# Kernel tuning notes

Hardware: AMD Instinct MI355X
Metric: run time of the kernel (lower is better)

Reference implementation:

```python
import jax, jax.numpy as jnp
import numpy as np

B, L, H, D = 1, 2048, 24, 128
BLKQ = BLKK = 64
TOPK_RATIO = 0.5


def setup_inputs() -> dict:
    key = jax.random.key(0)
    kq, kk, kv, kw = jax.random.split(key, 4)
    q = jax.random.normal(kq, (B, L, H, D), jnp.float32)
    k = jax.random.normal(kk, (B, L, H, D), jnp.float32)
    v = jax.random.normal(kv, (B, L, H, D), jnp.float32)
    proj_w = jax.random.normal(kw, (D, D), jnp.float32) * 0.02  # nn.Linear weight (out,in)
    proj_b = jnp.zeros((D,), jnp.float32)
    return {"query": q, "key": k, "value": v, "proj_w": proj_w, "proj_b": proj_b}


def _block_sparse_attention(q, k, v, scale):
    # q,k,v: (B,H,L,D). Block-mean pooled QK scores pick top-k key blocks per query block.
    Nq, Nk = L // BLKQ, L // BLKK
    topk = max(1, int(Nk * TOPK_RATIO))  # real_topk
    qb = q.reshape(B, H, Nq, BLKQ, D).mean(axis=3)          # (B,H,Nq,D)
    kb = k.reshape(B, H, Nk, BLKK, D).mean(axis=3)          # (B,H,Nk,D)
    blk_scores = jnp.einsum('bhqd,bhkd->bhqk', qb, kb)      # pooled block map
    _, lut = jax.lax.top_k(blk_scores, topk)                # (B,H,Nq,topk) selected key blocks
    kblk = k.reshape(B, H, Nk, BLKK, D)
    vblk = v.reshape(B, H, Nk, BLKK, D)
    idx = lut.reshape(B, H, Nq * topk, 1, 1)
    kg = jnp.take_along_axis(kblk, idx, axis=2).reshape(B, H, Nq, topk * BLKK, D)
    vg = jnp.take_along_axis(vblk, idx, axis=2).reshape(B, H, Nq, topk * BLKK, D)
    qr = q.reshape(B, H, Nq, BLKQ, D)
    scores = jnp.einsum('bhqid,bhqjd->bhqij', qr, kg) * scale  # (B,H,Nq,BLKQ,topk*BLKK)
    attn = jax.nn.softmax(scores, axis=-1)
    o = jnp.einsum('bhqij,bhqjd->bhqid', attn, vg)
    return o.reshape(B, H, L, D)


def _linear_attention(q, k, v):
    # feature_map='softmax' over the head dim
    ql = jax.nn.softmax(q, axis=-1)
    kl = jax.nn.softmax(k, axis=-1)
    kvsum = jnp.einsum('bhld,bhle->bhde', kl, v)            # K^T V  (B,H,D,D)
    ksum = kl.sum(axis=2)                                    # (B,H,D)
    num = jnp.einsum('bhld,bhde->bhle', ql, kvsum)
    den = 1e-5 + jnp.einsum('bhld,bhd->bhl', ql, ksum)[..., None]
    return num / den


def reference(query, key, value, proj_w, proj_b):
    q = jnp.swapaxes(query, 1, 2)  # (B,H,L,D)
    k = jnp.swapaxes(key, 1, 2)
    v = jnp.swapaxes(value, 1, 2)
    scale = D ** -0.5  # softmax_scale = head_size**-0.5
    o_s = _block_sparse_attention(q, k, v, scale)
    o_l = _linear_attention(q, k, v)
    o_l = o_l @ proj_w.T + proj_b  # learnable fusion projection
    out = jnp.swapaxes(o_s + o_l, 1, 2)  # back to (B,L,H,D)
    return out
```

## Files before the change

kernel.cpp:

```cpp
#include <hip/hip_runtime.h>
#include <math.h>

#define HH 24
#define LLEN 2048
#define DD 128
#define BLK 64
#define NBLK 32
#define TOPK 16
#define NCHUNK 16

typedef __attribute__((ext_vector_type(8))) short bf16x8;
typedef __attribute__((ext_vector_type(4))) float f32x4;

typedef unsigned int u32_g __attribute__((address_space(1)));
typedef unsigned int u32_l __attribute__((address_space(3)));

__device__ __forceinline__ unsigned short f2bf(float f) {
    unsigned u = __builtin_bit_cast(unsigned, f);
    unsigned r = (u + 0x7FFFu + ((u >> 16) & 1u)) >> 16;
    return (unsigned short)r;
}
__device__ __forceinline__ float bf2f(unsigned short b) {
    unsigned u = ((unsigned)b) << 16;
    return __builtin_bit_cast(float, u);
}
__device__ __forceinline__ void gload16(unsigned short* lds, const unsigned short* g) {
    __builtin_amdgcn_global_load_lds((const u32_g*)g, (u32_l*)lds, 16, 0, 0);
}

__global__ __launch_bounds__(256) void convert_pool(
    const float* __restrict__ q, const float* __restrict__ k, const float* __restrict__ v,
    unsigned short* __restrict__ kb16, unsigned short* __restrict__ vt16,
    float* __restrict__ qb, float* __restrict__ kb)
{
    const int nb = blockIdx.x, h = blockIdx.y;
    const int l0 = nb * BLK;
    const int tid = threadIdx.x;
    __shared__ unsigned short vt_s[DD * BLK];

    {
        const int r = tid >> 2, c0 = (tid & 3) * 4;
        const float* kp = k + ((size_t)(l0 + r) * HH + h) * DD + c0 * 8;
        unsigned short* krow = kb16 + ((size_t)h * LLEN + l0 + r) * DD;
        #pragma unroll
        for (int j = 0; j < 4; ++j) {
            float4 a = *(const float4*)(kp + j * 8);
            float4 c = *(const float4*)(kp + j * 8 + 4);
            unsigned short tmp[8] = {f2bf(a.x), f2bf(a.y), f2bf(a.z), f2bf(a.w),
                                     f2bf(c.x), f2bf(c.y), f2bf(c.z), f2bf(c.w)};
            const int chunk = (c0 + j) ^ (r & 7);
            *(bf16x8*)&krow[chunk * 8] = *(bf16x8*)tmp;
        }
    }
    {
        const int kp2 = tid >> 3, dgb = tid & 7;
        const float* v0p = v + ((size_t)(l0 + kp2 * 2) * HH + h) * DD;
        const float* v1p = v0p + (size_t)HH * DD;
        #pragma unroll
        for (int j2 = 0; j2 < 4; ++j2) {
            const int d0 = dgb * 4 + j2 * 32;
            float4 a = *(const float4*)(v0p + d0);
            float4 c = *(const float4*)(v1p + d0);
            float a4[4] = {a.x, a.y, a.z, a.w}, c4[4] = {c.x, c.y, c.z, c.w};
            #pragma unroll
            for (int i = 0; i < 4; ++i) {
                unsigned pak = (unsigned)f2bf(a4[i]) | ((unsigned)f2bf(c4[i]) << 16);
                const int d = d0 + i;
                const int chunk = (kp2 >> 2) ^ (d & 7);
                *(unsigned*)&vt_s[d * BLK + chunk * 8 + (kp2 & 3) * 2] = pak;
            }
        }
    }
    __syncthreads();
    {
        bf16x8* dstv = (bf16x8*)(vt16 + (size_t)(h * NBLK + nb) * DD * BLK);
        const bf16x8* srcv = (const bf16x8*)vt_s;
        #pragma unroll
        for (int j = 0; j < 4; ++j) dstv[tid * 4 + j] = srcv[tid * 4 + j];
    }
    __syncthreads();
    {
        float* ps = (float*)vt_s;
        const int d = tid & 127, half = tid >> 7;
        const size_t rs = (size_t)HH * DD;
        const float* qp = q + ((size_t)(l0 + half * 32) * HH + h) * DD + d;
        const float* kp = k + ((size_t)(l0 + half * 32) * HH + h) * DD + d;
        float sq = 0.f, sk = 0.f;
        #pragma unroll 8
        for (int i = 0; i < 32; ++i) { sq += qp[i * rs]; sk += kp[i * rs]; }
        ps[half * 128 + d] = sq;
        ps[256 + half * 128 + d] = sk;
        __syncthreads();
        if (half == 0) {
            qb[((size_t)h * NBLK + nb) * DD + d] = ps[d] + ps[128 + d];
            kb[((size_t)h * NBLK + nb) * DD + d] = ps[256 + d] + ps[384 + d];
        }
    }
}

__global__ __launch_bounds__(256) void topk_kernel(
    const float* __restrict__ qb, const float* __restrict__ kb, int* __restrict__ lut)
{
    const int h = blockIdx.x;
    __shared__ float kb_s[NBLK][DD];
    __shared__ float sc[NBLK][NBLK];
    const int tid = threadIdx.x;
    for (int f = tid; f < NBLK * DD / 4; f += 256)
        ((float4*)kb_s)[f] = ((const float4*)(kb + (size_t)h * NBLK * DD))[f];
    __syncthreads();
    for (int p = tid; p < NBLK * NBLK; p += 256) {
        const int iq = p >> 5, ik = p & 31;
        const float4* qr4 = (const float4*)(qb + ((size_t)h * NBLK + iq) * DD);
        const float4* kr4 = (const float4*)&kb_s[ik][0];
        float s = 0.f;
        for (int dq = 0; dq < DD / 4; ++dq) {
            float4 a = qr4[dq], b = kr4[dq];
            s += a.x * b.x + a.y * b.y + a.z * b.z + a.w * b.w;
        }
        sc[iq][ik] = s;
    }
    __syncthreads();
    if (tid < NBLK) {
        const int iq = tid;
        for (int t = 0; t < TOPK; ++t) {
            float bv = -1e30f; int bi = 0;
            for (int j = 0; j < NBLK; ++j) {
                float s = sc[iq][j];
                if (s > bv) { bv = s; bi = j; }
            }
            lut[((size_t)h * NBLK + iq) * TOPK + t] = bi;
            sc[iq][bi] = -1e30f;
        }
    }
}

__global__ __launch_bounds__(256, 2) void kv_mfma(
    const float* __restrict__ k, const unsigned short* __restrict__ vt16,
    float* __restrict__ kvp, float* __restrict__ ksp)
{
    const int h = blockIdx.x, c = blockIdx.y;
    __shared__ unsigned short klT[DD * DD];
    const int tid = threadIdx.x;
    const int quad = tid >> 3, dpart = tid & 7;
    const int d0 = dpart * 16;
    const int wid = tid >> 6, lane = tid & 63;
    const int l15 = lane & 15, g = lane >> 4;

    f32x4 acc[2][8];
    #pragma unroll
    for (int mi = 0; mi < 2; ++mi)
        #pragma unroll
        for (int nt = 0; nt < 8; ++nt) acc[mi][nt] = (f32x4){0.f, 0.f, 0.f, 0.f};
    float ksa[16];
    #pragma unroll
    for (int j = 0; j < 16; ++j) ksa[j] = 0.f;

    const int l0 = c * DD;
    {
        const int lr = quad * 4;
        float rows[4][16];
        #pragma unroll
        for (int i = 0; i < 4; ++i) {
            const float4* kp4 = (const float4*)(k + ((size_t)(l0 + lr + i) * HH + h) * DD + d0);
            #pragma unroll
            for (int t4 = 0; t4 < 4; ++t4) {
                float4 x = kp4[t4];
                rows[i][t4 * 4 + 0] = x.x; rows[i][t4 * 4 + 1] = x.y;
                rows[i][t4 * 4 + 2] = x.z; rows[i][t4 * 4 + 3] = x.w;
            }
        }
        #pragma unroll
        for (int i = 0; i < 4; ++i) {
            float mx = -1e30f;
            #pragma unroll
            for (int j = 0; j < 16; ++j) mx = fmaxf(mx, rows[i][j]);
            mx = fmaxf(mx, __shfl_xor(mx, 1));
            mx = fmaxf(mx, __shfl_xor(mx, 2));
            mx = fmaxf(mx, __shfl_xor(mx, 4));
            float s = 0.f;
            #pragma unroll
            for (int j = 0; j < 16; ++j) { rows[i][j] = __expf(rows[i][j] - mx); s += rows[i][j]; }
            s += __shfl_xor(s, 1);
            s += __shfl_xor(s, 2);
            s += __shfl_xor(s, 4);
            const float rinv = 1.0f / s;
            #pragma unroll
            for (int j = 0; j < 16; ++j) { rows[i][j] *= rinv; ksa[j] += rows[i][j]; }
        }
        #pragma unroll
        for (int j = 0; j < 16; ++j) {
            const int d = d0 + j;
            unsigned long long pk =
                (unsigned long long)f2bf(rows[0][j]) |
                ((unsigned long long)f2bf(rows[1][j]) << 16) |
                ((unsigned long long)f2bf(rows[2][j]) << 32) |
                ((unsigned long long)f2bf(rows[3][j]) << 48);
            const int chunk = (quad >> 1) ^ (d & 7);
            *(unsigned long long*)&klT[d * DD + chunk * 8 + (quad & 1) * 4] = pk;
        }
    }
    __syncthreads();
    const int bkt = c * 2;
    #pragma unroll
    for (int ks = 0; ks < 4; ++ks) {
        bf16x8 af[2];
        #pragma unroll
        for (int mi = 0; mi < 2; ++mi) {
            const int d = (wid * 2 + mi) * 16 + l15;
            const int chunk = (ks * 4 + g) ^ (d & 7);
            af[mi] = *(const bf16x8*)&klT[d * DD + chunk * 8];
        }
        const int s = ks * 4 + g;
        const int kt = bkt + (s >> 3);
        #pragma unroll
        for (int nt = 0; nt < 8; ++nt) {
            const int e = nt * 16 + l15;
            const int cc = (s & 7) ^ (e & 7);
            bf16x8 bf = *(const bf16x8*)&vt16[((size_t)(h * NBLK + kt) * DD + e) * BLK + cc * 8];
            acc[0][nt] = __builtin_amdgcn_mfma_f32_16x16x32_bf16(af[0], bf, acc[0][nt], 0, 0, 0);
            acc[1][nt] = __builtin_amdgcn_mfma_f32_16x16x32_bf16(af[1], bf, acc[1][nt], 0, 0, 0);
        }
    }
    float* op = kvp + ((size_t)h * NCHUNK + c) * DD * DD;
    #pragma unroll
    for (int mi = 0; mi < 2; ++mi)
        #pragma unroll
        for (int nt = 0; nt < 8; ++nt)
            #pragma unroll
            for (int r = 0; r < 4; ++r)
                op[(size_t)((wid * 2 + mi) * 16 + g * 4 + r) * DD + nt * 16 + l15] = acc[mi][nt][r];
    #pragma unroll
    for (int j = 0; j < 16; ++j) {
        ksa[j] += __shfl_xor(ksa[j], 8);
        ksa[j] += __shfl_xor(ksa[j], 16);
        ksa[j] += __shfl_xor(ksa[j], 32);
    }
    if ((lane >> 3) == 0) {
        float* kp2 = ksp + (((size_t)h * NCHUNK + c) * 4 + wid) * DD + d0;
        #pragma unroll
        for (int j = 0; j < 16; ++j) kp2[j] = ksa[j];
    }
}

__global__ __launch_bounds__(256) void reduce_M(
    const float* __restrict__ kvp, const float* __restrict__ ksp,
    const float* __restrict__ W, unsigned short* __restrict__ Mt,
    float* __restrict__ ksumf)
{
    const int h = blockIdx.x, rb = blockIdx.y;
    __shared__ float kv_s[32][DD];
    const int tid = threadIdx.x;
    for (int f4 = tid; f4 < 32 * DD / 4; f4 += 256) {
        float4 s = make_float4(0.f, 0.f, 0.f, 0.f);
        #pragma unroll
        for (int cc = 0; cc < NCHUNK; ++cc) {
            float4 x = ((const float4*)(kvp + ((size_t)h * NCHUNK + cc) * DD * DD
                                        + (size_t)rb * 32 * DD))[f4];
            s.x += x.x; s.y += x.y; s.z += x.z; s.w += x.w;
        }
        ((float4*)kv_s)[f4] = s;
    }
    if (rb == 0 && tid < DD) {
        float s = 0.f;
        #pragma unroll
        for (int p = 0; p < NCHUNK * 4; ++p)
            s += ksp[((size_t)h * NCHUNK * 4 + p) * DD + tid];
        ksumf[(size_t)h * DD + tid] = s;
    }
    __syncthreads();
    const int e = tid & 127, dh = tid >> 7;
    float accm[16];
    #pragma unroll
    for (int i = 0; i < 16; ++i) accm[i] = 0.f;
    const float4* wr4 = (const float4*)(W + (size_t)e * DD);
    for (int c4 = 0; c4 < DD / 4; ++c4) {
        const float4 wv = wr4[c4];
        #pragma unroll
        for (int i = 0; i < 16; ++i) {
            const float4 kv4 = ((const float4*)&kv_s[dh * 16 + i][0])[c4];
            accm[i] += kv4.x * wv.x + kv4.y * wv.y + kv4.z * wv.z + kv4.w * wv.w;
        }
    }
    unsigned short* mp = Mt + (size_t)h * DD * DD + (size_t)e * DD + rb * 32 + dh * 16;
    #pragma unroll
    for (int ii = 0; ii < 16; ii += 2) {
        unsigned pk = (unsigned)f2bf(accm[ii]) | ((unsigned)f2bf(accm[ii + 1]) << 16);
        *(unsigned*)&mp[ii] = pk;
    }
}

__global__ __launch_bounds__(256, 2) void sla_attn(
    const float* __restrict__ q, const unsigned short* __restrict__ kb16,
    const unsigned short* __restrict__ vt16, const int* __restrict__ lut,
    const unsigned short* __restrict__ Mt, const float* __restrict__ ksumf,
    const float* __restrict__ pb, float* __restrict__ out)
{
    const int b = blockIdx.x;
    const int slot = b >> 3;
    const int h = (b & 7) + 8 * (slot >> 5);
    const int nq = slot & 31;

    __shared__ unsigned short Ks[2][BLK * DD];
    __shared__ unsigned short Vt[2][DD * BLK];
    __shared__ unsigned short Ps[4 * 16 * BLK];

    const int tid = threadIdx.x;
    const int wid = tid >> 6, lane = tid & 63;
    const int l15 = lane & 15, g = lane >> 4;
    const int q0 = wid * 16;

    bf16x8 qhi[4], qlo[4];
    {
        const float scale = 0.08838834764831845f;
        const int qrow = nq * BLK + q0 + l15;
        const float* qp = q + ((size_t)qrow * HH + h) * DD;
        #pragma unroll
        for (int ks = 0; ks < 4; ++ks) {
            const int d0 = ks * 32 + g * 8;
            float4 a = *(const float4*)(qp + d0);
            float4 c = *(const float4*)(qp + d0 + 4);
            float vv[8] = {a.x, a.y, a.z, a.w, c.x, c.y, c.z, c.w};
            #pragma unroll
            for (int j = 0; j < 8; ++j) {
                float s = vv[j] * scale;
                unsigned short hi = f2bf(s);
                float lo = s - bf2f(hi);
                qhi[ks][j] = (short)hi;
                qlo[ks][j] = (short)f2bf(lo);
            }
        }
    }

    f32x4 Oacc[8];
    #pragma unroll
    for (int nt = 0; nt < 8; ++nt) Oacc[nt] = (f32x4){0.f, 0.f, 0.f, 0.f};
    float m_run = -1e30f, l_run = 0.f;

    const int* lrow = lut + ((size_t)h * NBLK + nq) * TOPK;

    {
        const int kbI = lrow[0];
        const unsigned short* kg = kb16 + ((size_t)h * LLEN + (size_t)kbI * BLK) * DD;
        const unsigned short* vg = vt16 + (size_t)(h * NBLK + kbI) * DD * BLK;
        #pragma unroll
        for (int i = 0; i < 4; ++i) {
            const int is = wid * 4 + i;
            gload16(&Ks[0][is * 512], kg + is * 512 + lane * 8);
            gload16(&Vt[0][is * 512], vg + is * 512 + lane * 8);
        }
    }
    __syncthreads();

    for (int it = 0; it < TOPK; ++it) {
        const int cur = it & 1;
        if (it + 1 < TOPK) {
            const int kbN = lrow[it + 1];
            const unsigned short* kg = kb16 + ((size_t)h * LLEN + (size_t)kbN * BLK) * DD;
            const unsigned short* vg = vt16 + (size_t)(h * NBLK + kbN) * DD * BLK;
            #pragma unroll
            for (int i = 0; i < 4; ++i) {
                const int is = wid * 4 + i;
                gload16(&Ks[cur ^ 1][is * 512], kg + is * 512 + lane * 8);
                gload16(&Vt[cur ^ 1][is * 512], vg + is * 512 + lane * 8);
            }
        }
        const unsigned short* KsC = &Ks[cur][0];
        const unsigned short* VtC = &Vt[cur][0];

        f32x4 sacc[4];
        #pragma unroll
        for (int mt = 0; mt < 4; ++mt) sacc[mt] = (f32x4){0.f, 0.f, 0.f, 0.f};
        #pragma unroll
        for (int ks = 0; ks < 4; ++ks) {
            #pragma unroll
            for (int mt = 0; mt < 4; ++mt) {
                const int row = mt * 16 + l15;
                const int chunk = (ks * 4 + g) ^ (row & 7);
                bf16x8 kf = *(const bf16x8*)&KsC[row * DD + chunk * 8];
                sacc[mt] = __builtin_amdgcn_mfma_f32_16x16x32_bf16(kf, qhi[ks], sacc[mt], 0, 0, 0);
                sacc[mt] = __builtin_amdgcn_mfma_f32_16x16x32_bf16(kf, qlo[ks], sacc[mt], 0, 0, 0);
            }
        }

        float sv[16];
        #pragma unroll
        for (int mt = 0; mt < 4; ++mt)
            #pragma unroll
            for (int r = 0; r < 4; ++r) sv[mt * 4 + r] = sacc[mt][r];
        float mx = -1e30f;
        #pragma unroll
        for (int i = 0; i < 16; ++i) mx = fmaxf(mx, sv[i]);
        mx = fmaxf(mx, __shfl_xor(mx, 16));
        mx = fmaxf(mx, __shfl_xor(mx, 32));
        const float mnew = fmaxf(m_run, mx);
        const float alpha = __expf(m_run - mnew);
        float ssum = 0.f;
        #pragma unroll
        for (int i = 0; i < 16; ++i) { sv[i] = __expf(sv[i] - mnew); ssum += sv[i]; }
        ssum += __shfl_xor(ssum, 16);
        ssum += __shfl_xor(ssum, 32);
        l_run = l_run * alpha + ssum;
        m_run = mnew;

        {
            unsigned short* pw = Ps + wid * (16 * BLK) + l15 * BLK;
            #pragma unroll
            for (int mt = 0; mt < 4; ++mt) {
                #pragma unroll
                for (int pr = 0; pr < 2; ++pr) {
                    const int key = mt * 16 + g * 4 + pr * 2;
                    unsigned pak = (unsigned)f2bf(sv[mt * 4 + pr * 2])
                                 | ((unsigned)f2bf(sv[mt * 4 + pr * 2 + 1]) << 16);
                    const int chunk = (key >> 3) ^ (l15 & 7);
                    *(unsigned*)&pw[chunk * 8 + (key & 7)] = pak;
                }
            }
        }

        {
            float ar[4];
            #pragma unroll
            for (int r = 0; r < 4; ++r) ar[r] = __shfl(alpha, g * 4 + r);
            #pragma unroll
            for (int nt = 0; nt < 8; ++nt) {
                Oacc[nt][0] *= ar[0]; Oacc[nt][1] *= ar[1];
                Oacc[nt][2] *= ar[2]; Oacc[nt][3] *= ar[3];
            }
            const unsigned short* prd = Ps + wid * (16 * BLK) + l15 * BLK;
            #pragma unroll
            for (int ks2 = 0; ks2 < 2; ++ks2) {
                const int pch = (g + 4 * ks2) ^ (l15 & 7);
                bf16x8 pa = *(const bf16x8*)&prd[pch * 8];
                #pragma unroll
                for (int nt = 0; nt < 8; ++nt) {
                    const int drow = nt * 16 + l15;
                    const int vch = (g + 4 * ks2) ^ (drow & 7);
                    bf16x8 vf = *(const bf16x8*)&VtC[drow * BLK + vch * 8];
                    Oacc[nt] = __builtin_amdgcn_mfma_f32_16x16x32_bf16(pa, vf, Oacc[nt], 0, 0, 0);
                }
            }
        }
        __syncthreads();
    }

    float qv[32];
    {
        const float iscale = 11.313708498984761f;
        #pragma unroll
        for (int ks = 0; ks < 4; ++ks)
            #pragma unroll
            for (int j = 0; j < 8; ++j)
                qv[ks * 8 + j] = (bf2f((unsigned short)qhi[ks][j])
                                + bf2f((unsigned short)qlo[ks][j])) * iscale;
    }
    float mx2 = -1e30f;
    #pragma unroll
    for (int j = 0; j < 32; ++j) mx2 = fmaxf(mx2, qv[j]);
    mx2 = fmaxf(mx2, __shfl_xor(mx2, 16));
    mx2 = fmaxf(mx2, __shfl_xor(mx2, 32));
    float s2 = 0.f;
    #pragma unroll
    for (int j = 0; j < 32; ++j) { qv[j] = __expf(qv[j] - mx2); s2 += qv[j]; }
    s2 += __shfl_xor(s2, 16);
    s2 += __shfl_xor(s2, 32);
    const float rinv = 1.0f / s2;
    float den = 0.f;
    bf16x8 af[4];
    {
        const float* ksb = ksumf + (size_t)h * DD;
        #pragma unroll
        for (int ks = 0; ks < 4; ++ks) {
            const int dd0 = ks * 32 + g * 8;
            float4 k0 = *(const float4*)(ksb + dd0);
            float4 k1 = *(const float4*)(ksb + dd0 + 4);
            float kk[8] = {k0.x, k0.y, k0.z, k0.w, k1.x, k1.y, k1.z, k1.w};
            #pragma unroll
            for (int j = 0; j < 8; ++j) {
                const float ql = qv[ks * 8 + j] * rinv;
                af[ks][j] = (short)f2bf(ql);
                den += ql * kk[j];
            }
        }
    }
    den += __shfl_xor(den, 16);
    den += __shfl_xor(den, 32);
    const float dinv = 1.0f / (1e-5f + den);

    f32x4 acc2[8];
    #pragma unroll
    for (int nt = 0; nt < 8; ++nt) acc2[nt] = (f32x4){0.f, 0.f, 0.f, 0.f};
    {
        const unsigned short* mrow = Mt + (size_t)h * DD * DD;
        #pragma unroll
        for (int ks = 0; ks < 4; ++ks) {
            #pragma unroll
            for (int nt = 0; nt < 8; ++nt) {
                bf16x8 bf = *(const bf16x8*)&mrow[(size_t)(nt * 16 + l15) * DD + (ks * 4 + g) * 8];
                acc2[nt] = __builtin_amdgcn_mfma_f32_16x16x32_bf16(af[ks], bf, acc2[nt], 0, 0, 0);
            }
        }
    }

    float bias[8];
    #pragma unroll
    for (int nt = 0; nt < 8; ++nt) bias[nt] = pb[nt * 16 + l15];
    #pragma unroll
    for (int r = 0; r < 4; ++r) {
        const float linv = 1.0f / __shfl(l_run, g * 4 + r);
        const float di = __shfl(dinv, g * 4 + r);
        const int grow = nq * BLK + q0 + g * 4 + r;
        float* dst = out + ((size_t)grow * HH + h) * DD + l15;
        #pragma unroll
        for (int nt = 0; nt < 8; ++nt)
            dst[nt * 16] = Oacc[nt][r] * linv + acc2[nt][r] * di + bias[nt];
    }
}

extern "C" void kernel_launch(void* const* d_in, const int* in_sizes, int n_in,
                              void* d_out, int out_size, void* d_ws, size_t ws_size,
                              hipStream_t stream)
{
    (void)in_sizes; (void)n_in; (void)out_size; (void)ws_size;
    const float* q  = (const float*)d_in[0];
    const float* k  = (const float*)d_in[1];
    const float* v  = (const float*)d_in[2];
    const float* pw = (const float*)d_in[3];
    const float* pb = (const float*)d_in[4];
    float* out = (float*)d_out;
    char* ws = (char*)d_ws;
    size_t off = 0;
    int*   lut   = (int*)(ws + off);   off += (size_t)HH * NBLK * TOPK * 4;
    float* qb    = (float*)(ws + off); off += (size_t)HH * NBLK * DD * 4;
    float* kb    = (float*)(ws + off); off += (size_t)HH * NBLK * DD * 4;
    float* kvp   = (float*)(ws + off); off += (size_t)HH * NCHUNK * DD * DD * 4;
    float* ksp   = (float*)(ws + off); off += (size_t)HH * NCHUNK * 4 * DD * 4;
    unsigned short* Mt = (unsigned short*)(ws + off); off += (size_t)HH * DD * DD * 2;
    float* ksumf = (float*)(ws + off); off += (size_t)HH * DD * 4;
    unsigned short* kb16 = (unsigned short*)(ws + off); off += (size_t)HH * LLEN * DD * 2;
    unsigned short* vt16 = (unsigned short*)(ws + off); off += (size_t)HH * LLEN * DD * 2;

    convert_pool<<<dim3(NBLK, HH), 256, 0, stream>>>(q, k, v, kb16, vt16, qb, kb);
    topk_kernel<<<HH, 256, 0, stream>>>(qb, kb, lut);
    kv_mfma<<<dim3(HH, NCHUNK), 256, 0, stream>>>(k, vt16, kvp, ksp);
    reduce_M<<<dim3(HH, 4), 256, 0, stream>>>(kvp, ksp, pw, Mt, ksumf);
    sla_attn<<<NBLK * HH, 256, 0, stream>>>(q, kb16, vt16, lut, Mt, ksumf, pb, out);
}
```

Baseline: 153.9 us.

## Restructure sparse attention to two 32-row warps with V read directly from global

The attention kernel drops from 4 waves of 16 query rows to 2 waves handling 32 rows each (two 16-row subtiles), which doubles register-level reuse of each K fragment. The V tile is no longer staged through shared memory; it is read straight from global memory in an unswizzled transposed layout, and the converter now writes vt16 unswizzled to match. K double-buffering uses manual vmcnt waits and raw barriers, and setprio hints are added around the MFMA blocks. This cuts LDS traffic and footprint, at the cost of more registers, fewer waves per block and uncoalesced global V reads that rely on the cache.

```diff
diff --git a/kernel.cpp b/kernel.cpp
--- a/kernel.cpp
+++ b/kernel.cpp
@@ -76,7 +76,11 @@
         bf16x8* dstv = (bf16x8*)(vt16 + (size_t)(h * NBLK + nb) * DD * BLK);
         const bf16x8* srcv = (const bf16x8*)vt_s;
         #pragma unroll
-        for (int j = 0; j < 4; ++j) dstv[tid * 4 + j] = srcv[tid * 4 + j];
+        for (int j = 0; j < 4; ++j) {
+            const int u = tid * 4 + j;
+            const int e = u >> 3, c = u & 7;
+            dstv[u] = srcv[e * 8 + (c ^ (e & 7))];
+        }
     }
     __syncthreads();
     {
@@ -215,7 +219,7 @@
         #pragma unroll
         for (int nt = 0; nt < 8; ++nt) {
             const int e = nt * 16 + l15;
-            const int cc = (s & 7) ^ (e & 7);
+            const int cc = s & 7;
             bf16x8 bf = *(const bf16x8*)&vt16[((size_t)(h * NBLK + kt) * DD + e) * BLK + cc * 8];
             acc[0][nt] = __builtin_amdgcn_mfma_f32_16x16x32_bf16(af[0], bf, acc[0][nt], 0, 0, 0);
             acc[1][nt] = __builtin_amdgcn_mfma_f32_16x16x32_bf16(af[1], bf, acc[1][nt], 0, 0, 0);
@@ -289,7 +293,7 @@
     }
 }
 
-__global__ __launch_bounds__(256, 2) void sla_attn(
+__global__ __launch_bounds__(128, 2) void sla_attn(
     const float* __restrict__ q, const unsigned short* __restrict__ kb16,
     const unsigned short* __restrict__ vt16, const int* __restrict__ lut,
     const unsigned short* __restrict__ Mt, const float* __restrict__ ksumf,
@@ -301,18 +305,17 @@
     const int nq = slot & 31;
 
     __shared__ unsigned short Ks[2][BLK * DD];
-    __shared__ unsigned short Vt[2][DD * BLK];
-    __shared__ unsigned short Ps[4 * 16 * BLK];
+    __shared__ unsigned short Ps[2][32 * BLK];
 
     const int tid = threadIdx.x;
     const int wid = tid >> 6, lane = tid & 63;
     const int l15 = lane & 15, g = lane >> 4;
-    const int q0 = wid * 16;
-
-    bf16x8 qhi[4], qlo[4];
-    {
+
+    bf16x8 qhi[2][4], qlo[2][4];
+    #pragma unroll
+    for (int st = 0; st < 2; ++st) {
         const float scale = 0.08838834764831845f;
-        const int qrow = nq * BLK + q0 + l15;
+        const int qrow = nq * BLK + wid * 32 + st * 16 + l15;
         const float* qp = q + ((size_t)qrow * HH + h) * DD;
         #pragma unroll
         for (int ks = 0; ks < 4; ++ks) {
@@ -325,85 +328,102 @@
                 float s = vv[j] * scale;
                 unsigned short hi = f2bf(s);
                 float lo = s - bf2f(hi);
-                qhi[ks][j] = (short)hi;
-                qlo[ks][j] = (short)f2bf(lo);
-            }
-        }
-    }
-
-    f32x4 Oacc[8];
-    #pragma unroll
-    for (int nt = 0; nt < 8; ++nt) Oacc[nt] = (f32x4){0.f, 0.f, 0.f, 0.f};
-    float m_run = -1e30f, l_run = 0.f;
+                qhi[st][ks][j] = (short)hi;
+                qlo[st][ks][j] = (short)f2bf(lo);
+            }
+        }
+    }
+
+    f32x4 Oacc[2][8];
+    #pragma unroll
+    for (int st = 0; st < 2; ++st)
+        #pragma unroll
+        for (int nt = 0; nt < 8; ++nt) Oacc[st][nt] = (f32x4){0.f, 0.f, 0.f, 0.f};
+    float m_run[2] = {-1e30f, -1e30f}, l_run[2] = {0.f, 0.f};
 
     const int* lrow = lut + ((size_t)h * NBLK + nq) * TOPK;
 
     {
-        const int kbI = lrow[0];
-        const unsigned short* kg = kb16 + ((size_t)h * LLEN + (size_t)kbI * BLK) * DD;
-        const unsigned short* vg = vt16 + (size_t)(h * NBLK + kbI) * DD * BLK;
-        #pragma unroll
-        for (int i = 0; i < 4; ++i) {
-            const int is = wid * 4 + i;
+        const int kb0 = lrow[0];
+        const unsigned short* kg = kb16 + ((size_t)h * LLEN + (size_t)kb0 * BLK) * DD;
+        #pragma unroll
+        for (int i = 0; i < 8; ++i) {
+            const int is = wid * 8 + i;
             gload16(&Ks[0][is * 512], kg + is * 512 + lane * 8);
-            gload16(&Vt[0][is * 512], vg + is * 512 + lane * 8);
-        }
-    }
-    __syncthreads();
+        }
+    }
 
     for (int it = 0; it < TOPK; ++it) {
         const int cur = it & 1;
+        const int kbI = lrow[it];
+        __builtin_amdgcn_s_barrier();
         if (it + 1 < TOPK) {
             const int kbN = lrow[it + 1];
             const unsigned short* kg = kb16 + ((size_t)h * LLEN + (size_t)kbN * BLK) * DD;
-            const unsigned short* vg = vt16 + (size_t)(h * NBLK + kbN) * DD * BLK;
-            #pragma unroll
-            for (int i = 0; i < 4; ++i) {
-                const int is = wid * 4 + i;
+            #pragma unroll
+            for (int i = 0; i < 8; ++i) {
+                const int is = wid * 8 + i;
                 gload16(&Ks[cur ^ 1][is * 512], kg + is * 512 + lane * 8);
-                gload16(&Vt[cur ^ 1][is * 512], vg + is * 512 + lane * 8);
-            }
-        }
-        const unsigned short* KsC = &Ks[cur][0];
-        const unsigned short* VtC = &Vt[cur][0];
-
-        f32x4 sacc[4];
-        #pragma unroll
-        for (int mt = 0; mt < 4; ++mt) sacc[mt] = (f32x4){0.f, 0.f, 0.f, 0.f};
+            }
+            asm volatile("s_waitcnt vmcnt(8)" ::: "memory");
+        } else {
+            asm volatile("s_waitcnt vmcnt(0)" ::: "memory");
+        }
+        __builtin_amdgcn_sched_barrier(0);
+        __builtin_amdgcn_s_barrier();
+        __builtin_amdgcn_sched_barrier(0);
+
+        f32x4 sacc[2][4];
+        #pragma unroll
+        for (int st = 0; st < 2; ++st)
+            #pragma unroll
+            for (int mt = 0; mt < 4; ++mt) sacc[st][mt] = (f32x4){0.f, 0.f, 0.f, 0.f};
+        __builtin_amdgcn_s_setprio(1);
         #pragma unroll
         for (int ks = 0; ks < 4; ++ks) {
             #pragma unroll
             for (int mt = 0; mt < 4; ++mt) {
                 const int row = mt * 16 + l15;
                 const int chunk = (ks * 4 + g) ^ (row & 7);
-                bf16x8 kf = *(const bf16x8*)&KsC[row * DD + chunk * 8];
-                sacc[mt] = __builtin_amdgcn_mfma_f32_16x16x32_bf16(kf, qhi[ks], sacc[mt], 0, 0, 0);
-                sacc[mt] = __builtin_amdgcn_mfma_f32_16x16x32_bf16(kf, qlo[ks], sacc[mt], 0, 0, 0);
-            }
-        }
-
-        float sv[16];
-        #pragma unroll
-        for (int mt = 0; mt < 4; ++mt)
-            #pragma unroll
-            for (int r = 0; r < 4; ++r) sv[mt * 4 + r] = sacc[mt][r];
-        float mx = -1e30f;
-        #pragma unroll
-        for (int i = 0; i < 16; ++i) mx = fmaxf(mx, sv[i]);
-        mx = fmaxf(mx, __shfl_xor(mx, 16));
-        mx = fmaxf(mx, __shfl_xor(mx, 32));
-        const float mnew = fmaxf(m_run, mx);
-        const float alpha = __expf(m_run - mnew);
-        float ssum = 0.f;
-        #pragma unroll
-        for (int i = 0; i < 16; ++i) { sv[i] = __expf(sv[i] - mnew); ssum += sv[i]; }
-        ssum += __shfl_xor(ssum, 16);
-        ssum += __shfl_xor(ssum, 32);
-        l_run = l_run * alpha + ssum;
-        m_run = mnew;
-
-        {
-            unsigned short* pw = Ps + wid * (16 * BLK) + l15 * BLK;
+                bf16x8 kf = *(const bf16x8*)&Ks[cur][row * DD + chunk * 8];
+                sacc[0][mt] = __builtin_amdgcn_mfma_f32_16x16x32_bf16(kf, qhi[0][ks], sacc[0][mt], 0, 0, 0);
+                sacc[0][mt] = __builtin_amdgcn_mfma_f32_16x16x32_bf16(kf, qlo[0][ks], sacc[0][mt], 0, 0, 0);
+                sacc[1][mt] = __builtin_amdgcn_mfma_f32_16x16x32_bf16(kf, qhi[1][ks], sacc[1][mt], 0, 0, 0);
+                sacc[1][mt] = __builtin_amdgcn_mfma_f32_16x16x32_bf16(kf, qlo[1][ks], sacc[1][mt], 0, 0, 0);
+            }
+        }
+        __builtin_amdgcn_s_setprio(0);
+
+        const unsigned short* vg = vt16 + (size_t)(h * NBLK + kbI) * DD * BLK;
+        bf16x8 vf0[8];
+        #pragma unroll
+        for (int nt = 0; nt < 8; ++nt)
+            vf0[nt] = *(const bf16x8*)&vg[(size_t)(nt * 16 + l15) * BLK + g * 8];
+
+        float alpha2[2];
+        #pragma unroll
+        for (int st = 0; st < 2; ++st) {
+            float sv[16];
+            #pragma unroll
+            for (int mt = 0; mt < 4; ++mt)
+                #pragma unroll
+                for (int r = 0; r < 4; ++r) sv[mt * 4 + r] = sacc[st][mt][r];
+            float mx = -1e30f;
+            #pragma unroll
+            for (int i = 0; i < 16; ++i) mx = fmaxf(mx, sv[i]);
+            mx = fmaxf(mx, __shfl_xor(mx, 16));
+            mx = fmaxf(mx, __shfl_xor(mx, 32));
+            const float mnew = fmaxf(m_run[st], mx);
+            const float alpha = __expf(m_run[st] - mnew);
+            float ssum = 0.f;
+            #pragma unroll
+            for (int i = 0; i < 16; ++i) { sv[i] = __expf(sv[i] - mnew); ssum += sv[i]; }
+            ssum += __shfl_xor(ssum, 16);
+            ssum += __shfl_xor(ssum, 32);
+            l_run[st] = l_run[st] * alpha + ssum;
+            m_run[st] = mnew;
+            alpha2[st] = alpha;
+            unsigned short* pw = &Ps[wid][(st * 16 + l15) * BLK];
             #pragma unroll
             for (int mt = 0; mt < 4; ++mt) {
                 #pragma unroll
@@ -418,56 +438,75 @@
         }
 
         {
-            float ar[4];
-            #pragma unroll
-            for (int r = 0; r < 4; ++r) ar[r] = __shfl(alpha, g * 4 + r);
-            #pragma unroll
-            for (int nt = 0; nt < 8; ++nt) {
-                Oacc[nt][0] *= ar[0]; Oacc[nt][1] *= ar[1];
-                Oacc[nt][2] *= ar[2]; Oacc[nt][3] *= ar[3];
-            }
-            const unsigned short* prd = Ps + wid * (16 * BLK) + l15 * BLK;
-            #pragma unroll
-            for (int ks2 = 0; ks2 < 2; ++ks2) {
-                const int pch = (g + 4 * ks2) ^ (l15 & 7);
-                bf16x8 pa = *(const bf16x8*)&prd[pch * 8];
+            #pragma unroll
+            for (int st = 0; st < 2; ++st) {
+                float ar[4];
+                #pragma unroll
+                for (int r = 0; r < 4; ++r) ar[r] = __shfl(alpha2[st], g * 4 + r);
                 #pragma unroll
                 for (int nt = 0; nt < 8; ++nt) {
-                    const int drow = nt * 16 + l15;
-                    const int vch = (g + 4 * ks2) ^ (drow & 7);
-                    bf16x8 vf = *(const bf16x8*)&VtC[drow * BLK + vch * 8];
-                    Oacc[nt] = __builtin_amdgcn_mfma_f32_16x16x32_bf16(pa, vf, Oacc[nt], 0, 0, 0);
+                    Oacc[st][nt][0] *= ar[0]; Oacc[st][nt][1] *= ar[1];
+                    Oacc[st][nt][2] *= ar[2]; Oacc[st][nt][3] *= ar[3];
                 }
             }
-        }
-        __syncthreads();
-    }
-
-    float qv[32];
-    {
-        const float iscale = 11.313708498984761f;
-        #pragma unroll
-        for (int ks = 0; ks < 4; ++ks)
-            #pragma unroll
-            for (int j = 0; j < 8; ++j)
-                qv[ks * 8 + j] = (bf2f((unsigned short)qhi[ks][j])
-                                + bf2f((unsigned short)qlo[ks][j])) * iscale;
-    }
-    float mx2 = -1e30f;
-    #pragma unroll
-    for (int j = 0; j < 32; ++j) mx2 = fmaxf(mx2, qv[j]);
-    mx2 = fmaxf(mx2, __shfl_xor(mx2, 16));
-    mx2 = fmaxf(mx2, __shfl_xor(mx2, 32));
-    float s2 = 0.f;
-    #pragma unroll
-    for (int j = 0; j < 32; ++j) { qv[j] = __expf(qv[j] - mx2); s2 += qv[j]; }
-    s2 += __shfl_xor(s2, 16);
-    s2 += __shfl_xor(s2, 32);
-    const float rinv = 1.0f / s2;
-    float den = 0.f;
-    bf16x8 af[4];
-    {
-        const float* ksb = ksumf + (size_t)h * DD;
+            bf16x8 vf1[8];
+            #pragma unroll
+            for (int nt = 0; nt < 8; ++nt)
+                vf1[nt] = *(const bf16x8*)&vg[(size_t)(nt * 16 + l15) * BLK + (4 + g) * 8];
+            const int pchunk0 = g ^ (l15 & 7);
+            bf16x8 paA = *(const bf16x8*)&Ps[wid][(l15) * BLK + pchunk0 * 8];
+            bf16x8 paB = *(const bf16x8*)&Ps[wid][(16 + l15) * BLK + pchunk0 * 8];
+            __builtin_amdgcn_s_setprio(1);
+            #pragma unroll
+            for (int nt = 0; nt < 8; ++nt) {
+                Oacc[0][nt] = __builtin_amdgcn_mfma_f32_16x16x32_bf16(paA, vf0[nt], Oacc[0][nt], 0, 0, 0);
+                Oacc[1][nt] = __builtin_amdgcn_mfma_f32_16x16x32_bf16(paB, vf0[nt], Oacc[1][nt], 0, 0, 0);
+            }
+            __builtin_amdgcn_s_setprio(0);
+            const int pchunk1 = (g + 4) ^ (l15 & 7);
+            paA = *(const bf16x8*)&Ps[wid][(l15) * BLK + pchunk1 * 8];
+            paB = *(const bf16x8*)&Ps[wid][(16 + l15) * BLK + pchunk1 * 8];
+            __builtin_amdgcn_s_setprio(1);
+            #pragma unroll
+            for (int nt = 0; nt < 8; ++nt) {
+                Oacc[0][nt] = __builtin_amdgcn_mfma_f32_16x16x32_bf16(paA, vf1[nt], Oacc[0][nt], 0, 0, 0);
+                Oacc[1][nt] = __builtin_amdgcn_mfma_f32_16x16x32_bf16(paB, vf1[nt], Oacc[1][nt], 0, 0, 0);
+            }
+            __builtin_amdgcn_s_setprio(0);
+        }
+    }
+
+    float bias[8];
+    #pragma unroll
+    for (int nt = 0; nt < 8; ++nt) bias[nt] = pb[nt * 16 + l15];
+    const unsigned short* mrow = Mt + (size_t)h * DD * DD;
+    const float* ksb = ksumf + (size_t)h * DD;
+
+    #pragma unroll
+    for (int st = 0; st < 2; ++st) {
+        float qv[32];
+        {
+            const float iscale = 11.313708498984761f;
+            #pragma unroll
+            for (int ks = 0; ks < 4; ++ks)
+                #pragma unroll
+                for (int j = 0; j < 8; ++j)
+                    qv[ks * 8 + j] = (bf2f((unsigned short)qhi[st][ks][j])
+                                    + bf2f((unsigned short)qlo[st][ks][j])) * iscale;
+        }
+        float mx2 = -1e30f;
+        #pragma unroll
+        for (int j = 0; j < 32; ++j) mx2 = fmaxf(mx2, qv[j]);
+        mx2 = fmaxf(mx2, __shfl_xor(mx2, 16));
+        mx2 = fmaxf(mx2, __shfl_xor(mx2, 32));
+        float s2 = 0.f;
+        #pragma unroll
+        for (int j = 0; j < 32; ++j) { qv[j] = __expf(qv[j] - mx2); s2 += qv[j]; }
+        s2 += __shfl_xor(s2, 16);
+        s2 += __shfl_xor(s2, 32);
+        const float rinv = 1.0f / s2;
+        float den = 0.f;
+        bf16x8 af[4];
         #pragma unroll
         for (int ks = 0; ks < 4; ++ks) {
             const int dd0 = ks * 32 + g * 8;
@@ -481,16 +520,13 @@
                 den += ql * kk[j];
             }
         }
-    }
-    den += __shfl_xor(den, 16);
-    den += __shfl_xor(den, 32);
-    const float dinv = 1.0f / (1e-5f + den);
-
-    f32x4 acc2[8];
-    #pragma unroll
-    for (int nt = 0; nt < 8; ++nt) acc2[nt] = (f32x4){0.f, 0.f, 0.f, 0.f};
-    {
-        const unsigned short* mrow = Mt + (size_t)h * DD * DD;
+        den += __shfl_xor(den, 16);
+        den += __shfl_xor(den, 32);
+        const float dinv = 1.0f / (1e-5f + den);
+
+        f32x4 acc2[8];
+        #pragma unroll
+        for (int nt = 0; nt < 8; ++nt) acc2[nt] = (f32x4){0.f, 0.f, 0.f, 0.f};
         #pragma unroll
         for (int ks = 0; ks < 4; ++ks) {
             #pragma unroll
@@ -499,20 +535,16 @@
                 acc2[nt] = __builtin_amdgcn_mfma_f32_16x16x32_bf16(af[ks], bf, acc2[nt], 0, 0, 0);
             }
         }
-    }
-
-    float bias[8];
-    #pragma unroll
-    for (int nt = 0; nt < 8; ++nt) bias[nt] = pb[nt * 16 + l15];
-    #pragma unroll
-    for (int r = 0; r < 4; ++r) {
-        const float linv = 1.0f / __shfl(l_run, g * 4 + r);
-        const float di = __shfl(dinv, g * 4 + r);
-        const int grow = nq * BLK + q0 + g * 4 + r;
-        float* dst = out + ((size_t)grow * HH + h) * DD + l15;
-        #pragma unroll
-        for (int nt = 0; nt < 8; ++nt)
-            dst[nt * 16] = Oacc[nt][r] * linv + acc2[nt][r] * di + bias[nt];
+        #pragma unroll
+        for (int r = 0; r < 4; ++r) {
+            const float linv = 1.0f / __shfl(l_run[st], g * 4 + r);
+            const float di = __shfl(dinv, g * 4 + r);
+            const int grow = nq * BLK + wid * 32 + st * 16 + g * 4 + r;
+            float* dst = out + ((size_t)grow * HH + h) * DD + l15;
+            #pragma unroll
+            for (int nt = 0; nt < 8; ++nt)
+                dst[nt * 16] = Oacc[st][nt][r] * linv + acc2[nt][r] * di + bias[nt];
+        }
     }
 }
 
@@ -543,5 +575,5 @@
     topk_kernel<<<HH, 256, 0, stream>>>(qb, kb, lut);
     kv_mfma<<<dim3(HH, NCHUNK), 256, 0, stream>>>(k, vt16, kvp, ksp);
     reduce_M<<<dim3(HH, 4), 256, 0, stream>>>(kvp, ksp, pw, Mt, ksumf);
-    sla_attn<<<NBLK * HH, 256, 0, stream>>>(q, kb16, vt16, lut, Mt, ksumf, pb, out);
-}
+    sla_attn<<<NBLK * HH, 128, 0, stream>>>(q, kb16, vt16, lut, Mt, ksumf, pb, out);
+}
```

Measured after the change: 197.6 us. 1.28x slower.

## Single-buffer K/V in LDS with staggered loads to raise occupancy

Applied to the files above, without the earlier changes.

Replaces the double-buffered K and V shared-memory tiles with single buffers. This cuts LDS per block roughly in half and raises the launch-bounds occupancy hint from 2 to 4 blocks per CU. To keep loads overlapped, V for the current block is fetched during QK^T and the next K is fetched during softmax/PV, using split vmcnt waits and raw s_barrier. It also raises wave priority around the MFMA loops. The cost is tighter reliance on hand-placed waits and barriers for cross-wave LDS visibility, which could race, and less prefetch distance.

```diff
diff --git a/kernel.cpp b/kernel.cpp
--- a/kernel.cpp
+++ b/kernel.cpp
@@ -289,7 +289,7 @@
     }
 }
 
-__global__ __launch_bounds__(256, 2) void sla_attn(
+__global__ __launch_bounds__(256, 4) void sla_attn(
     const float* __restrict__ q, const unsigned short* __restrict__ kb16,
     const unsigned short* __restrict__ vt16, const int* __restrict__ lut,
     const unsigned short* __restrict__ Mt, const float* __restrict__ ksumf,
@@ -300,8 +300,8 @@
     const int h = (b & 7) + 8 * (slot >> 5);
     const int nq = slot & 31;
 
-    __shared__ unsigned short Ks[2][BLK * DD];
-    __shared__ unsigned short Vt[2][DD * BLK];
+    __shared__ unsigned short Ks[BLK * DD];
+    __shared__ unsigned short Vt[DD * BLK];
     __shared__ unsigned short Ps[4 * 16 * BLK];
 
     const int tid = threadIdx.x;
@@ -339,46 +339,54 @@
     const int* lrow = lut + ((size_t)h * NBLK + nq) * TOPK;
 
     {
-        const int kbI = lrow[0];
-        const unsigned short* kg = kb16 + ((size_t)h * LLEN + (size_t)kbI * BLK) * DD;
-        const unsigned short* vg = vt16 + (size_t)(h * NBLK + kbI) * DD * BLK;
+        const int kb0 = lrow[0];
+        const unsigned short* kg = kb16 + ((size_t)h * LLEN + (size_t)kb0 * BLK) * DD;
         #pragma unroll
         for (int i = 0; i < 4; ++i) {
             const int is = wid * 4 + i;
-            gload16(&Ks[0][is * 512], kg + is * 512 + lane * 8);
-            gload16(&Vt[0][is * 512], vg + is * 512 + lane * 8);
-        }
-    }
-    __syncthreads();
+            gload16(&Ks[is * 512], kg + is * 512 + lane * 8);
+        }
+    }
 
     for (int it = 0; it < TOPK; ++it) {
-        const int cur = it & 1;
+        const int kbI = lrow[it];
+        __builtin_amdgcn_s_barrier();
+        {
+            const unsigned short* vg = vt16 + (size_t)(h * NBLK + kbI) * DD * BLK;
+            #pragma unroll
+            for (int i = 0; i < 4; ++i) {
+                const int is = wid * 4 + i;
+                gload16(&Vt[is * 512], vg + is * 512 + lane * 8);
+            }
+        }
+        asm volatile("s_waitcnt vmcnt(4)" ::: "memory");
+        __builtin_amdgcn_sched_barrier(0);
+
+        f32x4 sacc[4];
+        #pragma unroll
+        for (int mt = 0; mt < 4; ++mt) sacc[mt] = (f32x4){0.f, 0.f, 0.f, 0.f};
+        __builtin_amdgcn_s_setprio(1);
+        #pragma unroll
+        for (int ks = 0; ks < 4; ++ks) {
+            #pragma unroll
+            for (int mt = 0; mt < 4; ++mt) {
+                const int row = mt * 16 + l15;
+                const int chunk = (ks * 4 + g) ^ (row & 7);
+                bf16x8 kf = *(const bf16x8*)&Ks[row * DD + chunk * 8];
+                sacc[mt] = __builtin_amdgcn_mfma_f32_16x16x32_bf16(kf, qhi[ks], sacc[mt], 0, 0, 0);
+                sacc[mt] = __builtin_amdgcn_mfma_f32_16x16x32_bf16(kf, qlo[ks], sacc[mt], 0, 0, 0);
+            }
+        }
+        __builtin_amdgcn_s_setprio(0);
+
+        __builtin_amdgcn_s_barrier();
         if (it + 1 < TOPK) {
             const int kbN = lrow[it + 1];
             const unsigned short* kg = kb16 + ((size_t)h * LLEN + (size_t)kbN * BLK) * DD;
-            const unsigned short* vg = vt16 + (size_t)(h * NBLK + kbN) * DD * BLK;
             #pragma unroll
             for (int i = 0; i < 4; ++i) {
                 const int is = wid * 4 + i;
-                gload16(&Ks[cur ^ 1][is * 512], kg + is * 512 + lane * 8);
-                gload16(&Vt[cur ^ 1][is * 512], vg + is * 512 + lane * 8);
-            }
-        }
-        const unsigned short* KsC = &Ks[cur][0];
-        const unsigned short* VtC = &Vt[cur][0];
-
-        f32x4 sacc[4];
-        #pragma unroll
-        for (int mt = 0; mt < 4; ++mt) sacc[mt] = (f32x4){0.f, 0.f, 0.f, 0.f};
-        #pragma unroll
-        for (int ks = 0; ks < 4; ++ks) {
-            #pragma unroll
-            for (int mt = 0; mt < 4; ++mt) {
-                const int row = mt * 16 + l15;
-                const int chunk = (ks * 4 + g) ^ (row & 7);
-                bf16x8 kf = *(const bf16x8*)&KsC[row * DD + chunk * 8];
-                sacc[mt] = __builtin_amdgcn_mfma_f32_16x16x32_bf16(kf, qhi[ks], sacc[mt], 0, 0, 0);
-                sacc[mt] = __builtin_amdgcn_mfma_f32_16x16x32_bf16(kf, qlo[ks], sacc[mt], 0, 0, 0);
+                gload16(&Ks[is * 512], kg + is * 512 + lane * 8);
             }
         }
 
@@ -417,6 +425,13 @@
             }
         }
 
+        if (it + 1 < TOPK) {
+            asm volatile("s_waitcnt vmcnt(4)" ::: "memory");
+        } else {
+            asm volatile("s_waitcnt vmcnt(0)" ::: "memory");
+        }
+        __builtin_amdgcn_sched_barrier(0);
+
         {
             float ar[4];
             #pragma unroll
@@ -431,16 +446,17 @@
             for (int ks2 = 0; ks2 < 2; ++ks2) {
                 const int pch = (g + 4 * ks2) ^ (l15 & 7);
                 bf16x8 pa = *(const bf16x8*)&prd[pch * 8];
+                __builtin_amdgcn_s_setprio(1);
                 #pragma unroll
                 for (int nt = 0; nt < 8; ++nt) {
                     const int drow = nt * 16 + l15;
                     const int vch = (g + 4 * ks2) ^ (drow & 7);
-                    bf16x8 vf = *(const bf16x8*)&VtC[drow * BLK + vch * 8];
+                    bf16x8 vf = *(const bf16x8*)&Vt[drow * BLK + vch * 8];
                     Oacc[nt] = __builtin_amdgcn_mfma_f32_16x16x32_bf16(pa, vf, Oacc[nt], 0, 0, 0);
                 }
-            }
-        }
-        __syncthreads();
+                __builtin_amdgcn_s_setprio(0);
+            }
+        }
     }
 
     float qv[32];
```

Measured after the change: 160.9 us. +4.6%, slower.
